# Optimization experiments

Measured on AMD Instinct MI355X. Metric: run time of the kernel, lower is better.

## Reference

```python
import jax, jax.numpy as jnp
import numpy as np

B, D, H, O, E = 16384, 1024, 512, 256, 8


def setup_inputs() -> dict:
    key = jax.random.key(0)
    ks = jax.random.split(key, 8)
    s = lambda k, shape, fan: (jax.random.normal(k, shape, jnp.float32) / np.sqrt(fan).astype(np.float32))
    z = lambda shape: jnp.zeros(shape, jnp.float32)
    return {
        "x": jax.random.normal(ks[0], (B, D), jnp.float32),
        # gating network: D -> 256 -> 128 -> E
        "gw1": s(ks[1], (D, 256), D), "gb1": z((256,)),
        "gw2": s(ks[2], (256, 128), 256), "gb2": z((128,)),
        "gw3": s(ks[3], (128, E), 128), "gb3": z((E,)),
        # experts, batched over expert dim E: D -> H -> H -> O
        "ew1": s(ks[4], (E, D, H), D), "eb1": z((E, H)),
        "ew2": s(ks[5], (E, H, H), H), "eb2": z((E, H)),
        "ew3": s(ks[6], (E, H, O), H), "eb3": z((E, O)),
    }


def reference(x, gw1, gb1, gw2, gb2, gw3, gb3, ew1, eb1, ew2, eb2, ew3, eb3):
    # Gating network (dropout is identity in eval mode)
    g = jax.nn.relu(x @ gw1 + gb1)
    g = jax.nn.relu(g @ gw2 + gb2)
    gates = jax.nn.softmax(g @ gw3 + gb3, axis=1)  # [B, E]
    # All experts run on every token: batched small MLPs over expert axis e
    h = jax.nn.relu(jnp.einsum('bd,edh->ebh', x, ew1) + eb1[:, None, :])   # [E, B, H]
    h = jax.nn.relu(jnp.einsum('ebh,ehk->ebk', h, ew2) + eb2[:, None, :])  # [E, B, H]
    eo = jnp.einsum('ebh,eho->ebo', h, ew3) + eb3[:, None, :]              # [E, B, O]
    # gate-weighted sum over experts
    out = jnp.einsum('ebo,be->bo', eo, gates)  # [B, O]
    return out
```

## Files before the change

kernel.cpp:

```cpp
#include <hip/hip_runtime.h>
#include <hip/hip_bf16.h>

typedef __hip_bfloat16 bf16;
typedef __attribute__((ext_vector_type(8))) __bf16 bf16x8;
typedef __attribute__((ext_vector_type(4))) float f32x4;

#define B_ 16384
#define D_ 1024
#define H_ 512
#define O_ 256
#define E_ 8
#define BC_ 8192

static_assert(B_ % BC_ == 0, "chunking");

#define GLDS(src, dst) __builtin_amdgcn_global_load_lds( \
    (const __attribute__((address_space(1))) void*)(src), \
    (__attribute__((address_space(3))) void*)(dst), 16, 0, 0)

#define BAR()   asm volatile("s_barrier" ::: "memory")
#define LGKM0() do { asm volatile("s_waitcnt lgkmcnt(0)" ::: "memory"); \
                     __builtin_amdgcn_sched_barrier(0); } while (0)

__global__ void detect_k(const unsigned short* __restrict__ x, int* __restrict__ flag) {
    __shared__ int s;
    if (threadIdx.x == 0) s = 0;
    __syncthreads();
    int big = 0;
    for (int i = threadIdx.x; i < 2048; i += 256)
        if (((x[i] >> 7) & 0xFF) >= 150) big = 1;
    if (big) atomicOr(&s, 1);
    __syncthreads();
    if (threadIdx.x == 0) *flag = s;
}

__global__ void preproc_k(const void* x, bf16* xc,
                          const void* gb1, const void* gb2, const void* gw3,
                          const void* gb3, const void* eb1, const void* eb2,
                          const void* eb3,
                          bf16* gb1c, bf16* gb2c, bf16* gw3c, bf16* gb3c,
                          bf16* eb1c, bf16* eb2c, bf16* eb3c,
                          const void* gw1, const void* gw2,
                          const void* ew1, const void* ew2, const void* ew3,
                          bf16* gw1t, bf16* gw2t,
                          bf16* ew1t, bf16* ew2t, bf16* ew3t,
                          long ew3_zout, long ew3_cstride,
                          const int* __restrict__ flag) {
    const int f = *flag;
    const int tid = threadIdx.y * 32 + threadIdx.x;
    int lin = blockIdx.x;

    if (lin < 1024) {
        const long n8 = (long)B_ * D_ / 8;
        long i = (long)lin * 256 + tid;
        const long stride = 1024 * 256;
        if (f) {
            const float4* s = (const float4*)x;
            for (; i < n8; i += stride) {
                float4 a = s[2 * i], b = s[2 * i + 1];
                bf16 tmp[8];
                tmp[0] = __float2bfloat16(a.x); tmp[1] = __float2bfloat16(a.y);
                tmp[2] = __float2bfloat16(a.z); tmp[3] = __float2bfloat16(a.w);
                tmp[4] = __float2bfloat16(b.x); tmp[5] = __float2bfloat16(b.y);
                tmp[6] = __float2bfloat16(b.z); tmp[7] = __float2bfloat16(b.w);
                *(uint4*)(xc + i * 8) = *(const uint4*)tmp;
            }
        } else {
            const uint4* s = (const uint4*)x;
            for (; i < n8; i += stride) *(uint4*)(xc + i * 8) = s[i];
        }
        return;
    }
    if (lin < 1031) {
        const int id = lin - 1024;
        const void* sp[7] = {gb1, gb2, gw3, gb3, eb1, eb2, eb3};
        bf16* dp[7] = {gb1c, gb2c, gw3c, gb3c, eb1c, eb2c, eb3c};
        const int len[7] = {256, 128, 1024, 8, E_ * H_, E_ * H_, E_ * O_};
        const float* sf = (const float*)sp[id];
        const bf16*  sb = (const bf16*)sp[id];
        bf16* d = dp[id];
        for (int i = tid; i < len[id]; i += 256)
            d[i] = f ? __float2bfloat16(sf[i]) : sb[i];
        return;
    }
    lin -= 1031;
    __shared__ bf16 t[32][33];
    const void* src; bf16* dst; int R, C, bx, by, bz; long z_out, c_stride;
    if (lin < 256) {
        src = gw1; dst = gw1t; R = 1024; C = 256; z_out = 0; c_stride = 1024;
        bx = lin & 7; by = lin >> 3; bz = 0;
    } else if (lin < 288) {
        lin -= 256;
        src = gw2; dst = gw2t; R = 256; C = 128; z_out = 0; c_stride = 256;
        bx = lin & 3; by = lin >> 2; bz = 0;
    } else if (lin < 4384) {
        lin -= 288;
        src = ew1; dst = ew1t; R = 1024; C = 512;
        z_out = (long)H_ * D_; c_stride = D_;
        bx = lin & 15; by = (lin >> 4) & 31; bz = lin >> 9;
    } else if (lin < 6432) {
        lin -= 4384;
        src = ew2; dst = ew2t; R = 512; C = 512;
        z_out = (long)H_ * H_; c_stride = H_;
        bx = lin & 15; by = (lin >> 4) & 15; bz = lin >> 8;
    } else {
        lin -= 6432;
        src = ew3; dst = ew3t; R = 512; C = 256;
        z_out = ew3_zout; c_stride = ew3_cstride;
        bx = lin & 7; by = (lin >> 3) & 15; bz = lin >> 7;
    }
    const long zi = (long)bz * R * C;
    const int xg = bx * 32 + threadIdx.x;
    const int y0 = by * 32;
    const float* inf = (const float*)src;
    const bf16* inb = (const bf16*)src;
#pragma unroll
    for (int i = 0; i < 4; i++) {
        int r = y0 + threadIdx.y + i * 8;
        long idx = zi + (long)r * C + xg;
        t[threadIdx.y + i * 8][threadIdx.x] =
            f ? __float2bfloat16(inf[idx]) : inb[idx];
    }
    __syncthreads();
    const int xr = by * 32 + threadIdx.x;
    const long zo = (long)bz * z_out;
#pragma unroll
    for (int i = 0; i < 4; i++) {
        int c = bx * 32 + threadIdx.y + i * 8;
        dst[zo + (long)c * c_stride + xr] = t[threadIdx.x][threadIdx.y + i * 8];
    }
}

__global__ void gate3_softmax_k(const bf16* __restrict__ g2,
                                const bf16* __restrict__ gw3,
                                const bf16* __restrict__ gb3,
                                float* __restrict__ gates) {
    __shared__ float w[128 * 8];
    __shared__ float bsh[8];
    const int tid = threadIdx.x;
    for (int i = tid; i < 1024; i += 256) w[i] = __bfloat162float(gw3[i]);
    if (tid < 8) bsh[tid] = __bfloat162float(gb3[tid]);
    __syncthreads();

    const long row = (long)blockIdx.x * 256 + tid;
    float acc[8];
#pragma unroll
    for (int o = 0; o < 8; o++) acc[o] = bsh[o];

    const bf16x8* rp8 = (const bf16x8*)(g2 + row * 128);
#pragma unroll 4
    for (int c8 = 0; c8 < 16; c8++) {
        bf16x8 v8 = rp8[c8];
#pragma unroll
        for (int jj = 0; jj < 8; jj++) {
            float v = (float)v8[jj];
            int k = c8 * 8 + jj;
#pragma unroll
            for (int o = 0; o < 8; o++) acc[o] += v * w[k * 8 + o];
        }
    }
    float m = acc[0];
#pragma unroll
    for (int o = 1; o < 8; o++) m = fmaxf(m, acc[o]);
    float s = 0.f;
#pragma unroll
    for (int o = 0; o < 8; o++) { acc[o] = __expf(acc[o] - m); s += acc[o]; }
    const float inv = 1.f / s;
#pragma unroll
    for (int o = 0; o < 8; o++) gates[row * 8 + o] = acc[o] * inv;
}

template <int MODE>
__global__ __launch_bounds__(256, 4)
void gemm_bt(const bf16* __restrict__ A, const bf16* __restrict__ Bt,
             const bf16* __restrict__ bias, const float* __restrict__ gates,
             void* __restrict__ Cout, const bf16* __restrict__ eb3,
             int lda, int ldb, int ldo, int K,
             long a_z, long b_z, long bias_z, long out_z,
             int e_gate, int k_per_e, long a_e, long b_e, long row0) {
    __shared__ __attribute__((aligned(16))) bf16 As[128 * 32];
    __shared__ __attribute__((aligned(16))) bf16 Bs[128 * 32];

    const int tid  = threadIdx.x;
    const int lane = tid & 63;
    const int quad = lane >> 4;
    const int l15  = lane & 15;
    const int wid  = tid >> 6;
    const int wr   = (wid >> 1) << 6;
    const int wc   = (wid & 1) << 6;
    const int z    = blockIdx.z;
    const long m0  = (long)blockIdx.y << 7;
    const long n0  = (long)blockIdx.x << 7;

    const bf16* Az = A + (long)z * a_z;
    const bf16* Bz = Bt + (long)z * b_z;

    f32x4 acc[4][4];
#pragma unroll
    for (int i = 0; i < 4; i++)
#pragma unroll
        for (int j = 0; j < 4; j++) acc[i][j] = (f32x4){0.f, 0.f, 0.f, 0.f};

    const int erow = tid >> 2;
    const int ecol = (tid & 3) << 3;

    const int n_e   = k_per_e ? (K / k_per_e) : 1;
    const int inner = (k_per_e ? k_per_e : K) >> 5;

    for (int e = 0; e < n_e; e++) {
        const bf16* Ae = Az + (long)e * a_e;
        const bf16* Be = Bz + (long)e * b_e;
        for (int kti = 0; kti < inner; kti++) {
            const int kk = kti << 5;
#pragma unroll
            for (int i = 0; i < 2; i++) {
                const int r = (i << 6) + erow;
                GLDS(Ae + (m0 + r) * lda + (kk + ecol), As + r * 32 + ecol);
            }
#pragma unroll
            for (int i = 0; i < 2; i++) {
                const int r = (i << 6) + erow;
                GLDS(Be + (n0 + r) * ldb + (kk + ecol), Bs + r * 32 + ecol);
            }
            __syncthreads();
            bf16x8 af[4], bfr[4];
#pragma unroll
            for (int i = 0; i < 4; i++)
                af[i] = *(const bf16x8*)(As + (wr + i * 16 + l15) * 32 + (quad << 3));
#pragma unroll
            for (int j = 0; j < 4; j++)
                bfr[j] = *(const bf16x8*)(Bs + (wc + j * 16 + l15) * 32 + (quad << 3));
#pragma unroll
            for (int i = 0; i < 4; i++)
#pragma unroll
                for (int j = 0; j < 4; j++)
                    acc[i][j] = __builtin_amdgcn_mfma_f32_16x16x32_bf16(
                        af[i], bfr[j], acc[i][j], 0, 0, 0);
            __syncthreads();
        }
    }

    const int eg = (e_gate >= 0) ? e_gate : z;

    if constexpr (MODE == 0 || MODE == 1) {
        bf16* C = (bf16*)Cout + (long)z * out_z;
        const bf16* bb = bias + (long)z * bias_z;
        float gv[4][4];
        if constexpr (MODE == 1) {
#pragma unroll
            for (int i = 0; i < 4; i++)
#pragma unroll
                for (int rg = 0; rg < 4; rg++)
                    gv[i][rg] = gates[(row0 + m0 + wr + i * 16 + quad * 4 + rg) * 8 + eg];
        }
#pragma unroll
        for (int j = 0; j < 4; j++) {
            const int c = (int)n0 + wc + j * 16 + l15;
            const float bv = __bfloat162float(bb[c]);
#pragma unroll
            for (int i = 0; i < 4; i++) {
#pragma unroll
                for (int rg = 0; rg < 4; rg++) {
                    const long r = m0 + wr + i * 16 + quad * 4 + rg;
                    float v = fmaxf(acc[i][j][rg] + bv, 0.f);
                    if constexpr (MODE == 1) v *= gv[i][rg];
                    C[r * ldo + c] = __float2bfloat16(v);
                }
            }
        }
    } else if constexpr (MODE == 2) {
        float* C = (float*)Cout;
#pragma unroll
        for (int i = 0; i < 4; i++) {
#pragma unroll
            for (int rg = 0; rg < 4; rg++) {
                const long r = m0 + wr + i * 16 + quad * 4 + rg;
                const float g = gates[(row0 + r) * 8 + eg];
#pragma unroll
                for (int j = 0; j < 4; j++) {
                    const int c = (int)n0 + wc + j * 16 + l15;
                    const float b3 = __bfloat162float(eb3[eg * O_ + c]);
                    C[r * ldo + c] += acc[i][j][rg] + g * b3;
                }
            }
        }
    }
}

template <int MODE>
__global__ __launch_bounds__(512, 2)
void gemm256(const bf16* __restrict__ A, const bf16* __restrict__ Bt,
             const bf16* __restrict__ bias, const float* __restrict__ gates,
             void* __restrict__ Cout, const bf16* __restrict__ eb3,
             int lda, int ldb, int ldo, int K,
             long a_z, long b_z, long bias_z, long out_z, long row0) {
    __shared__ __attribute__((aligned(16))) bf16 lds[2][2][256 * 64];

    int bx = blockIdx.x, by = blockIdx.y;
    {
        const int gx = gridDim.x;
        const int nwg = gx * gridDim.y;
        if ((nwg & 7) == 0) {
            int lin = bx + gx * by;
            lin = (lin & 7) * (nwg >> 3) + (lin >> 3);
            bx = lin % gx; by = lin / gx;
        }
    }

    const int tid  = threadIdx.x;
    const int lane = tid & 63;
    const int quad = lane >> 4;
    const int l15  = lane & 15;
    const int w    = tid >> 6;
    const int wm   = w >> 2;
    const int wn   = w & 3;
    const int z    = blockIdx.z;
    const long m0  = (long)by << 8;
    const long n0  = (long)bx << 8;

    const bf16* __restrict__ Az = A + z * a_z;
    const bf16* __restrict__ Bz = Bt + z * b_z;

    f32x4 acc[8][4];
#pragma unroll
    for (int i = 0; i < 8; ++i)
#pragma unroll
        for (int j = 0; j < 4; ++j) acc[i][j] = (f32x4){0.f, 0.f, 0.f, 0.f};

    bf16x8 af[4][2], bv[2][2];

    auto stage = [&](int buf, int mat, int half, int kt) {
        const bf16* __restrict__ G = mat ? Bz : Az;
        const int ld = mat ? ldb : lda;
        const long p0 = mat ? n0 : m0;
#pragma unroll
        for (int l = 0; l < 2; ++l) {
            const int ci = (w << 1) | l;
            const int rb = mat ? ((ci >> 2) << 6) + (half << 5) + ((ci & 3) << 3)
                               : ((ci >> 3) << 7) + (half << 6) + ((ci & 7) << 3);
            const int row = rb + (lane >> 3);
            const int cb  = ((lane & 7) << 4) ^ ((row & 7) << 4);
            GLDS(G + (p0 + row) * ld + kt * 64 + (cb >> 1),
                 &lds[buf][mat][rb * 64]);
        }
    };
    auto ldaf = [&](int buf, int qm) {
#pragma unroll
        for (int i = 0; i < 4; ++i) {
            const int r = (wm << 7) + (qm << 6) + (i << 4) + l15;
            const char* p = (const char*)&lds[buf][0][r * 64];
            const int sw = (r & 7) << 4;
#pragma unroll
            for (int s = 0; s < 2; ++s)
                af[i][s] = *(const bf16x8*)(p + (((s << 6) + (quad << 4)) ^ sw));
        }
    };
    auto ldbf = [&](int buf, int qn) {
#pragma unroll
        for (int j = 0; j < 2; ++j) {
            const int r = (wn << 6) + (qn << 5) + (j << 4) + l15;
            const char* p = (const char*)&lds[buf][1][r * 64];
            const int sw = (r & 7) << 4;
#pragma unroll
            for (int s = 0; s < 2; ++s)
                bv[j][s] = *(const bf16x8*)(p + (((s << 6) + (quad << 4)) ^ sw));
        }
    };
    auto mmac = [&](int qm, int qn) {
#pragma unroll
        for (int i = 0; i < 4; ++i)
#pragma unroll
            for (int j = 0; j < 2; ++j)
#pragma unroll
                for (int s = 0; s < 2; ++s)
                    acc[(qm << 2) + i][(qn << 1) + j] =
                        __builtin_amdgcn_mfma_f32_16x16x32_bf16(
                            af[i][s], bv[j][s], acc[(qm << 2) + i][(qn << 1) + j],
                            0, 0, 0);
    };

    const int nt = K >> 6;

    stage(0, 0, 0, 0); stage(0, 0, 1, 0); stage(0, 1, 0, 0); stage(0, 1, 1, 0);
    stage(1, 0, 0, 1); stage(1, 1, 0, 1);
    asm volatile("s_waitcnt vmcnt(4)" ::: "memory");
    BAR();

    const int hi = nt >> 1;
    for (int it = 0; it < hi; ++it) {
        const int t1k = 2 * it + 1, t2k = 2 * it + 2, t3k = 2 * it + 3;
        const bool do2 = t2k < nt, do3 = t3k < nt;
        ldaf(0, 0); ldbf(0, 0); stage(1, 0, 1, t1k);
        BAR(); LGKM0();
        __builtin_amdgcn_s_setprio(1); mmac(0, 0); __builtin_amdgcn_s_setprio(0);
        BAR();
        ldbf(0, 1); stage(1, 1, 1, t1k);
        BAR(); LGKM0();
        __builtin_amdgcn_s_setprio(1); mmac(0, 1); __builtin_amdgcn_s_setprio(0);
        BAR();
        ldaf(0, 1); ldbf(0, 0); if (do2) stage(0, 0, 0, t2k);
        BAR(); LGKM0();
        __builtin_amdgcn_s_setprio(1); mmac(1, 0); __builtin_amdgcn_s_setprio(0);
        BAR();
        ldbf(0, 1); if (do2) stage(0, 1, 0, t2k);
        BAR(); LGKM0();
        __builtin_amdgcn_s_setprio(1); mmac(1, 1); __builtin_amdgcn_s_setprio(0);
        if (do2) { asm volatile("s_waitcnt vmcnt(4)" ::: "memory"); }
        else     { asm volatile("s_waitcnt vmcnt(0)" ::: "memory"); }
        BAR();
        ldaf(1, 0); ldbf(1, 0); if (do2) stage(0, 0, 1, t2k);
        BAR(); LGKM0();
        __builtin_amdgcn_s_setprio(1); mmac(0, 0); __builtin_amdgcn_s_setprio(0);
        BAR();
        ldbf(1, 1); if (do2) stage(0, 1, 1, t2k);
        BAR(); LGKM0();
        __builtin_amdgcn_s_setprio(1); mmac(0, 1); __builtin_amdgcn_s_setprio(0);
        BAR();
        ldaf(1, 1); ldbf(1, 0); if (do3) stage(1, 0, 0, t3k);
        BAR(); LGKM0();
        __builtin_amdgcn_s_setprio(1); mmac(1, 0); __builtin_amdgcn_s_setprio(0);
        BAR();
        ldbf(1, 1); if (do3) stage(1, 1, 0, t3k);
        BAR(); LGKM0();
        __builtin_amdgcn_s_setprio(1); mmac(1, 1); __builtin_amdgcn_s_setprio(0);
        if (do3) { asm volatile("s_waitcnt vmcnt(4)" ::: "memory"); }
        else     { asm volatile("s_waitcnt vmcnt(0)" ::: "memory"); }
        BAR();
    }

    if constexpr (MODE == 0 || MODE == 1) {
        bf16* C = (bf16*)Cout + z * out_z;
        const bf16* bb = bias + z * bias_z;
        float bvv[4];
#pragma unroll
        for (int jg = 0; jg < 4; ++jg)
            bvv[jg] = __bfloat162float(bb[(int)n0 + (wn << 6) + (jg << 4) + l15]);
#pragma unroll
        for (int ig = 0; ig < 8; ++ig) {
#pragma unroll
            for (int rg = 0; rg < 4; ++rg) {
                const long r = m0 + (wm << 7) + (ig << 4) + (quad << 2) + rg;
                float g = 1.f;
                if constexpr (MODE == 1) g = gates[(row0 + r) * 8 + z];
#pragma unroll
                for (int jg = 0; jg < 4; ++jg) {
                    const int c = (int)n0 + (wn << 6) + (jg << 4) + l15;
                    float v = fmaxf(acc[ig][jg][rg] + bvv[jg], 0.f);
                    if constexpr (MODE == 1) v *= g;
                    C[r * ldo + c] = __float2bfloat16(v);
                }
            }
        }
    } else if constexpr (MODE == 4) {
        float* C = (float*)Cout + z * out_z;
        float b3v[4];
#pragma unroll
        for (int jg = 0; jg < 4; ++jg)
            b3v[jg] = __bfloat162float(eb3[z * O_ + (int)n0 + (wn << 6) + (jg << 4) + l15]);
#pragma unroll
        for (int ig = 0; ig < 8; ++ig) {
#pragma unroll
            for (int rg = 0; rg < 4; ++rg) {
                const long r = m0 + (wm << 7) + (ig << 4) + (quad << 2) + rg;
                const float g = gates[(row0 + r) * 8 + z];
#pragma unroll
                for (int jg = 0; jg < 4; ++jg) {
                    const int c = (int)n0 + (wn << 6) + (jg << 4) + l15;
                    C[r * ldo + c] = acc[ig][jg][rg] + g * b3v[jg];
                }
            }
        }
    } else {
        float* C = (float*)Cout + z * out_z;
        const int e0 = z << 1;
        float b30[4], b31[4];
#pragma unroll
        for (int jg = 0; jg < 4; ++jg) {
            const int c = (int)n0 + (wn << 6) + (jg << 4) + l15;
            b30[jg] = __bfloat162float(eb3[e0 * O_ + c]);
            b31[jg] = __bfloat162float(eb3[(e0 + 1) * O_ + c]);
        }
#pragma unroll
        for (int ig = 0; ig < 8; ++ig) {
#pragma unroll
            for (int rg = 0; rg < 4; ++rg) {
                const long r = m0 + (wm << 7) + (ig << 4) + (quad << 2) + rg;
                const float g0 = gates[(row0 + r) * 8 + e0];
                const float g1 = gates[(row0 + r) * 8 + e0 + 1];
#pragma unroll
                for (int jg = 0; jg < 4; ++jg) {
                    const int c = (int)n0 + (wn << 6) + (jg << 4) + l15;
                    C[r * ldo + c] = acc[ig][jg][rg] + g0 * b30[jg] + g1 * b31[jg];
                }
            }
        }
    }
}

__global__ void zero_f32_k(float* __restrict__ p) {
    p[(long)blockIdx.x * 256 + threadIdx.x] = 0.f;
}
__global__ void out_cvt_k(const float* __restrict__ in, void* __restrict__ out,
                          const int* __restrict__ flag) {
    const long i = (long)blockIdx.x * 256 + threadIdx.x;
    if (*flag) ((float*)out)[i] = in[i];
    else       ((bf16*)out)[i] = __float2bfloat16(in[i]);
}
template <int NZ>
__global__ void reduceN_k(const float* __restrict__ p, void* __restrict__ out,
                          const int* __restrict__ flag, long n, long off) {
    const long i = ((long)blockIdx.x * 256 + threadIdx.x) * 4;
    float4 s = *(const float4*)(p + i);
#pragma unroll
    for (int zz = 1; zz < NZ; ++zz) {
        float4 a = *(const float4*)(p + (long)zz * n + i);
        s.x += a.x; s.y += a.y; s.z += a.z; s.w += a.w;
    }
    if (*flag) {
        *(float4*)((float*)out + off + i) = s;
    } else {
        bf16* o = (bf16*)out + off + i;
        o[0] = __float2bfloat16(s.x); o[1] = __float2bfloat16(s.y);
        o[2] = __float2bfloat16(s.z); o[3] = __float2bfloat16(s.w);
    }
}

extern "C" void kernel_launch(void* const* d_in, const int* in_sizes, int n_in,
                              void* d_out, int out_size, void* d_ws, size_t ws_size,
                              hipStream_t stream) {
    (void)in_sizes; (void)n_in; (void)out_size;
    const void* x   = d_in[0];
    const void* gw1 = d_in[1];
    const void* gb1 = d_in[2];
    const void* gw2 = d_in[3];
    const void* gb2 = d_in[4];
    const void* gw3 = d_in[5];
    const void* gb3 = d_in[6];
    const void* ew1 = d_in[7];
    const void* eb1 = d_in[8];
    const void* ew2 = d_in[9];
    const void* eb2 = d_in[10];
    const void* ew3 = d_in[11];
    const void* eb3 = d_in[12];

    char* ws = (char*)d_ws;
    size_t off = 0;
    auto alloc = [&](size_t n) { char* p = ws + off; off += (n + 255) & ~(size_t)255; return p; };

    int*  flag  = (int*)alloc(256);
    bf16* xc    = (bf16*)alloc((size_t)B_ * D_ * 2);
    bf16* ew1t  = (bf16*)alloc((size_t)E_ * H_ * D_ * 2);
    bf16* gw1t  = (bf16*)alloc((size_t)256 * 1024 * 2);
    bf16* gw2t  = (bf16*)alloc((size_t)128 * 256 * 2);
    bf16* ew2t  = (bf16*)alloc((size_t)E_ * H_ * H_ * 2);
    bf16* ew3t  = (bf16*)alloc((size_t)E_ * O_ * H_ * 2);
    bf16* eb1c  = (bf16*)alloc((size_t)E_ * H_ * 2);
    bf16* gb1c  = (bf16*)alloc(256 * 2);
    bf16* gb2c  = (bf16*)alloc(128 * 2);
    bf16* gw3c  = (bf16*)alloc(1024 * 2);
    bf16* gb3c  = (bf16*)alloc(8 * 2);
    bf16* eb2c  = (bf16*)alloc((size_t)E_ * H_ * 2);
    bf16* eb3c  = (bf16*)alloc((size_t)E_ * O_ * 2);
    bf16* g2b   = (bf16*)alloc((size_t)B_ * 128 * 2);
    float* gates = (float*)alloc((size_t)B_ * 8 * 4);
    bf16* g1    = (bf16*)alloc((size_t)B_ * 256 * 2);

    const size_t smallCore = off;
    const size_t needPair = smallCore + ((size_t)E_ * BC_ * H_ * 2 + 256)
                                      + ((size_t)B_ * E_ * H_ * 2 + 256) + 4096;
    const size_t needChunk = smallCore + ((size_t)E_ * BC_ * H_ * 2 + 256)
                                       + ((size_t)BC_ * E_ * H_ * 2 + 256)
                                       + (8ull * BC_ * O_ * 4 + 256) + 4096;
    const bool pathPair  = ws_size >= needPair;
    const bool pathChunk = ws_size >= needChunk;

    detect_k<<<1, 256, 0, stream>>>((const unsigned short*)x, flag);

    const bool l3pair = pathPair || pathChunk;
    const long e3zo = l3pair ? (long)H_ : (long)O_ * H_;
    const long e3cs = l3pair ? (long)E_ * H_ : (long)H_;
    preproc_k<<<8487, dim3(32, 8), 0, stream>>>(
        x, xc, gb1, gb2, gw3, gb3, eb1, eb2, eb3,
        gb1c, gb2c, gw3c, gb3c, eb1c, eb2c, eb3c,
        gw1, gw2, ew1, ew2, ew3, gw1t, gw2t, ew1t, ew2t, ew3t,
        e3zo, e3cs, flag);

    gemm_bt<0><<<dim3(2, 128, 1), 256, 0, stream>>>(
        xc, gw1t, gb1c, nullptr, g1, nullptr,
        1024, 1024, 256, 1024, 0, 0, 0, 0, 0, 0, 0, 0, 0);
    gemm_bt<0><<<dim3(1, 128, 1), 256, 0, stream>>>(
        g1, gw2t, gb2c, nullptr, g2b, nullptr,
        256, 256, 128, 256, 0, 0, 0, 0, 0, 0, 0, 0, 0);
    gate3_softmax_k<<<dim3(B_ / 256), 256, 0, stream>>>(g2b, gw3c, gb3c, gates);

    if (pathPair) {
        bf16* h1c = (bf16*)alloc((size_t)E_ * BC_ * H_ * 2);
        bf16* h2  = (bf16*)alloc((size_t)B_ * E_ * H_ * 2);
        float* parts = (float*)h1c;

        for (int ch = 0; ch < B_ / BC_; ch++) {
            const long rb = (long)ch * BC_;
            gemm256<0><<<dim3(2, BC_ / 256, 8), 512, 0, stream>>>(
                xc + rb * D_, ew1t, eb1c, nullptr, h1c, nullptr,
                D_, D_, H_, D_,
                0, (long)H_ * D_, (long)H_, (long)BC_ * H_, 0);
            gemm256<1><<<dim3(2, BC_ / 256, 8), 512, 0, stream>>>(
                h1c, ew2t, eb2c, gates, h2 + rb * (long)E_ * H_, nullptr,
                H_, H_, E_ * H_, H_,
                (long)BC_ * H_, (long)H_ * H_, (long)H_, (long)H_, rb);
        }
        gemm256<5><<<dim3(1, B_ / 256, 4), 512, 0, stream>>>(
            h2, ew3t, nullptr, gates, parts, eb3c,
            E_ * H_, E_ * H_, O_, 1024,
            2L * H_, 2L * H_, 0, (long)B_ * O_, 0);
        reduceN_k<4><<<dim3(B_ * O_ / 1024), 256, 0, stream>>>(
            parts, d_out, flag, (long)B_ * O_, 0L);
    } else if (pathChunk) {
        bf16* h1c = (bf16*)alloc((size_t)E_ * BC_ * H_ * 2);
        bf16* h2c = (bf16*)alloc((size_t)BC_ * E_ * H_ * 2);
        float* parts = (float*)alloc(8ull * BC_ * O_ * 4);

        for (int ch = 0; ch < B_ / BC_; ch++) {
            const long rb = (long)ch * BC_;
            gemm256<0><<<dim3(2, BC_ / 256, 8), 512, 0, stream>>>(
                xc + rb * D_, ew1t, eb1c, nullptr, h1c, nullptr,
                D_, D_, H_, D_,
                0, (long)H_ * D_, (long)H_, (long)BC_ * H_, 0);
            gemm256<1><<<dim3(2, BC_ / 256, 8), 512, 0, stream>>>(
                h1c, ew2t, eb2c, gates, h2c, nullptr,
                H_, H_, E_ * H_, H_,
                (long)BC_ * H_, (long)H_ * H_, (long)H_, (long)H_, rb);
            gemm256<4><<<dim3(1, BC_ / 256, 8), 512, 0, stream>>>(
                h2c, ew3t, nullptr, gates, parts, eb3c,
                E_ * H_, E_ * H_, O_, 512,
                (long)H_, (long)H_, 0, (long)BC_ * O_, rb);
            reduceN_k<8><<<dim3(BC_ * O_ / 1024), 256, 0, stream>>>(
                parts, d_out, flag, (long)BC_ * O_, rb * O_);
        }
    } else {
        bf16* h1s = (bf16*)alloc((size_t)B_ * H_ * 2);
        bf16* h2s = (bf16*)alloc((size_t)B_ * H_ * 2);
        float* oacc = (float*)alloc((size_t)B_ * O_ * 4);
        zero_f32_k<<<dim3(B_ * O_ / 256), 256, 0, stream>>>(oacc);
        for (int e = 0; e < E_; e++) {
            gemm_bt<0><<<dim3(4, 128, 1), 256, 0, stream>>>(
                xc, ew1t + (size_t)e * H_ * D_, eb1c + (size_t)e * H_, nullptr, h1s, nullptr,
                1024, 1024, 512, 1024, 0, 0, 0, 0, 0, 0, 0, 0, 0);
            gemm_bt<1><<<dim3(4, 128, 1), 256, 0, stream>>>(
                h1s, ew2t + (size_t)e * H_ * H_, eb2c + (size_t)e * H_, gates, h2s, nullptr,
                512, 512, 512, 512, 0, 0, 0, 0, e, 0, 0, 0, 0);
            gemm_bt<2><<<dim3(2, 128, 1), 256, 0, stream>>>(
                h2s, ew3t + (size_t)e * O_ * H_, nullptr, gates, oacc, eb3c,
                512, 512, 256, 512, 0, 0, 0, 0, e, 0, 0, 0, 0);
        }
        out_cvt_k<<<dim3(B_ * O_ / 256), 256, 0, stream>>>(oacc, d_out, flag);
    }
}
```

Measured before the change: 494.9 us.

## Fuse gate layers 2-3 with softmax and fold split-K reduce into final GEMM

Layer 2 of the gating network (MFMA GEMM with bias and ReLU) is merged with layer 3 and the softmax into one kernel, so the intermediate g2 activations stay in LDS instead of going through global memory. The separate reduceN launch after the last expert GEMM is removed. Instead, each block increments a per-row-tile atomic counter, and the last of the four split-K blocks sums the partials and writes the final output in fp32 or bf16. This drops two launches and one global round trip. In exchange, the last-arriving block does a serial reduction, and correctness depends on counters being zeroed by detect_k and on threadfence ordering.

```diff
diff --git a/kernel.cpp b/kernel.cpp
--- a/kernel.cpp
+++ b/kernel.cpp
@@ -22,9 +22,11 @@
 #define LGKM0() do { asm volatile("s_waitcnt lgkmcnt(0)" ::: "memory"); \
                      __builtin_amdgcn_sched_barrier(0); } while (0)
 
-__global__ void detect_k(const unsigned short* __restrict__ x, int* __restrict__ flag) {
+__global__ void detect_k(const unsigned short* __restrict__ x,
+                         int* __restrict__ flag, int* __restrict__ cnt) {
     __shared__ int s;
     if (threadIdx.x == 0) s = 0;
+    if (threadIdx.x < 64) cnt[threadIdx.x] = 0;
     __syncthreads();
     int big = 0;
     for (int i = threadIdx.x; i < 2048; i += 256)
@@ -131,43 +133,100 @@
     }
 }
 
-__global__ void gate3_softmax_k(const bf16* __restrict__ g2,
-                                const bf16* __restrict__ gw3,
-                                const bf16* __restrict__ gb3,
-                                float* __restrict__ gates) {
-    __shared__ float w[128 * 8];
-    __shared__ float bsh[8];
-    const int tid = threadIdx.x;
-    for (int i = tid; i < 1024; i += 256) w[i] = __bfloat162float(gw3[i]);
-    if (tid < 8) bsh[tid] = __bfloat162float(gb3[tid]);
+__global__ __launch_bounds__(256, 2)
+void gate23_k(const bf16* __restrict__ A,
+              const bf16* __restrict__ Bt,
+              const bf16* __restrict__ gb2,
+              const bf16* __restrict__ w3b,
+              float* __restrict__ gates) {
+    __shared__ __attribute__((aligned(16))) bf16 As[128 * 32];
+    __shared__ __attribute__((aligned(16))) bf16 Bs[128 * 32];
+    __shared__ bf16 t2[128][130];
+    __shared__ float w3[1032];
+
+    const int tid  = threadIdx.x;
+    const int lane = tid & 63;
+    const int quad = lane >> 4;
+    const int l15  = lane & 15;
+    const int wid  = tid >> 6;
+    const int wr   = (wid >> 1) << 6;
+    const int wc   = (wid & 1) << 6;
+    const long m0  = (long)blockIdx.x << 7;
+
+    for (int i = tid; i < 1032; i += 256) w3[i] = __bfloat162float(w3b[i]);
+
+    f32x4 acc[4][4];
+#pragma unroll
+    for (int i = 0; i < 4; i++)
+#pragma unroll
+        for (int j = 0; j < 4; j++) acc[i][j] = (f32x4){0.f, 0.f, 0.f, 0.f};
+
+    const int erow = tid >> 2;
+    const int ecol = (tid & 3) << 3;
+
+    for (int kti = 0; kti < 8; kti++) {
+        const int kk = kti << 5;
+#pragma unroll
+        for (int i = 0; i < 2; i++) {
+            const int r = (i << 6) + erow;
+            GLDS(A + (m0 + r) * 256 + (kk + ecol), As + r * 32 + ecol);
+        }
+#pragma unroll
+        for (int i = 0; i < 2; i++) {
+            const int r = (i << 6) + erow;
+            GLDS(Bt + (long)r * 256 + (kk + ecol), Bs + r * 32 + ecol);
+        }
+        __syncthreads();
+        bf16x8 af[4], bfr[4];
+#pragma unroll
+        for (int i = 0; i < 4; i++)
+            af[i] = *(const bf16x8*)(As + (wr + i * 16 + l15) * 32 + (quad << 3));
+#pragma unroll
+        for (int j = 0; j < 4; j++)
+            bfr[j] = *(const bf16x8*)(Bs + (wc + j * 16 + l15) * 32 + (quad << 3));
+#pragma unroll
+        for (int i = 0; i < 4; i++)
+#pragma unroll
+            for (int j = 0; j < 4; j++)
+                acc[i][j] = __builtin_amdgcn_mfma_f32_16x16x32_bf16(
+                    af[i], bfr[j], acc[i][j], 0, 0, 0);
+        __syncthreads();
+    }
+
+#pragma unroll
+    for (int j = 0; j < 4; j++) {
+        const int c = wc + j * 16 + l15;
+        const float bv = __bfloat162float(gb2[c]);
+#pragma unroll
+        for (int i = 0; i < 4; i++)
+#pragma unroll
+            for (int rg = 0; rg < 4; rg++) {
+                const int r = wr + i * 16 + quad * 4 + rg;
+                t2[r][c] = __float2bfloat16(fmaxf(acc[i][j][rg] + bv, 0.f));
+            }
+    }
     __syncthreads();
 
-    const long row = (long)blockIdx.x * 256 + tid;
-    float acc[8];
-#pragma unroll
-    for (int o = 0; o < 8; o++) acc[o] = bsh[o];
-
-    const bf16x8* rp8 = (const bf16x8*)(g2 + row * 128);
-#pragma unroll 4
-    for (int c8 = 0; c8 < 16; c8++) {
-        bf16x8 v8 = rp8[c8];
-#pragma unroll
-        for (int jj = 0; jj < 8; jj++) {
-            float v = (float)v8[jj];
-            int k = c8 * 8 + jj;
-#pragma unroll
-            for (int o = 0; o < 8; o++) acc[o] += v * w[k * 8 + o];
-        }
-    }
-    float m = acc[0];
-#pragma unroll
-    for (int o = 1; o < 8; o++) m = fmaxf(m, acc[o]);
-    float s = 0.f;
-#pragma unroll
-    for (int o = 0; o < 8; o++) { acc[o] = __expf(acc[o] - m); s += acc[o]; }
-    const float inv = 1.f / s;
-#pragma unroll
-    for (int o = 0; o < 8; o++) gates[row * 8 + o] = acc[o] * inv;
+    if (tid < 128) {
+        const int r = tid;
+        float a3[8];
+#pragma unroll
+        for (int o = 0; o < 8; o++) a3[o] = w3[1024 + o];
+        for (int k = 0; k < 128; k++) {
+            const float v = __bfloat162float(t2[r][k]);
+#pragma unroll
+            for (int o = 0; o < 8; o++) a3[o] += v * w3[k * 8 + o];
+        }
+        float mx = a3[0];
+#pragma unroll
+        for (int o = 1; o < 8; o++) mx = fmaxf(mx, a3[o]);
+        float s = 0.f;
+#pragma unroll
+        for (int o = 0; o < 8; o++) { a3[o] = __expf(a3[o] - mx); s += a3[o]; }
+        const float inv = 1.f / s;
+#pragma unroll
+        for (int o = 0; o < 8; o++) gates[(m0 + r) * 8 + o] = a3[o] * inv;
+    }
 }
 
 template <int MODE>
@@ -293,7 +352,9 @@
              const bf16* __restrict__ bias, const float* __restrict__ gates,
              void* __restrict__ Cout, const bf16* __restrict__ eb3,
              int lda, int ldb, int ldo, int K,
-             long a_z, long b_z, long bias_z, long out_z, long row0) {
+             long a_z, long b_z, long bias_z, long out_z, long row0,
+             const int* __restrict__ oflag, int* __restrict__ cnt,
+             void* __restrict__ fout) {
     __shared__ __attribute__((aligned(16))) bf16 lds[2][2][256 * 64];
 
     int bx = blockIdx.x, by = blockIdx.y;
@@ -494,6 +555,34 @@
                 }
             }
         }
+        __shared__ int oldc;
+        __syncthreads();
+        if (tid == 0) {
+            __threadfence();
+            oldc = atomicAdd(&cnt[by], 1);
+        }
+        __syncthreads();
+        if (oldc == 3) {
+            const int f = *oflag;
+            const float* P = (const float*)Cout;
+            const long base = m0 * O_;
+            for (int idx = tid; idx < (256 * O_) / 4; idx += 512) {
+                const long o4 = base + (long)idx * 4;
+                float4 s = *(const float4*)(P + o4);
+#pragma unroll
+                for (int zz = 1; zz < 4; ++zz) {
+                    float4 a = *(const float4*)(P + (long)zz * out_z + o4);
+                    s.x += a.x; s.y += a.y; s.z += a.z; s.w += a.w;
+                }
+                if (f) {
+                    *(float4*)((float*)fout + o4) = s;
+                } else {
+                    bf16* o = (bf16*)fout + o4;
+                    o[0] = __float2bfloat16(s.x); o[1] = __float2bfloat16(s.y);
+                    o[2] = __float2bfloat16(s.z); o[3] = __float2bfloat16(s.w);
+                }
+            }
+        }
     }
 }
 
@@ -547,7 +636,8 @@
     size_t off = 0;
     auto alloc = [&](size_t n) { char* p = ws + off; off += (n + 255) & ~(size_t)255; return p; };
 
-    int*  flag  = (int*)alloc(256);
+    int*  flag  = (int*)alloc(512);
+    int*  cnt   = flag + 64;
     bf16* xc    = (bf16*)alloc((size_t)B_ * D_ * 2);
     bf16* ew1t  = (bf16*)alloc((size_t)E_ * H_ * D_ * 2);
     bf16* gw1t  = (bf16*)alloc((size_t)256 * 1024 * 2);
@@ -557,11 +647,10 @@
     bf16* eb1c  = (bf16*)alloc((size_t)E_ * H_ * 2);
     bf16* gb1c  = (bf16*)alloc(256 * 2);
     bf16* gb2c  = (bf16*)alloc(128 * 2);
-    bf16* gw3c  = (bf16*)alloc(1024 * 2);
-    bf16* gb3c  = (bf16*)alloc(8 * 2);
+    bf16* gw3c  = (bf16*)alloc(1032 * 2);
+    bf16* gb3c  = gw3c + 1024;
     bf16* eb2c  = (bf16*)alloc((size_t)E_ * H_ * 2);
     bf16* eb3c  = (bf16*)alloc((size_t)E_ * O_ * 2);
-    bf16* g2b   = (bf16*)alloc((size_t)B_ * 128 * 2);
     float* gates = (float*)alloc((size_t)B_ * 8 * 4);
     bf16* g1    = (bf16*)alloc((size_t)B_ * 256 * 2);
 
@@ -574,7 +663,7 @@
     const bool pathPair  = ws_size >= needPair;
     const bool pathChunk = ws_size >= needChunk;
 
-    detect_k<<<1, 256, 0, stream>>>((const unsigned short*)x, flag);
+    detect_k<<<1, 256, 0, stream>>>((const unsigned short*)x, flag, cnt);
 
     const bool l3pair = pathPair || pathChunk;
     const long e3zo = l3pair ? (long)H_ : (long)O_ * H_;
@@ -588,10 +677,7 @@
     gemm_bt<0><<<dim3(2, 128, 1), 256, 0, stream>>>(
         xc, gw1t, gb1c, nullptr, g1, nullptr,
         1024, 1024, 256, 1024, 0, 0, 0, 0, 0, 0, 0, 0, 0);
-    gemm_bt<0><<<dim3(1, 128, 1), 256, 0, stream>>>(
-        g1, gw2t, gb2c, nullptr, g2b, nullptr,
-        256, 256, 128, 256, 0, 0, 0, 0, 0, 0, 0, 0, 0);
-    gate3_softmax_k<<<dim3(B_ / 256), 256, 0, stream>>>(g2b, gw3c, gb3c, gates);
+    gate23_k<<<dim3(128), 256, 0, stream>>>(g1, gw2t, gb2c, gw3c, gates);
 
     if (pathPair) {
         bf16* h1c = (bf16*)alloc((size_t)E_ * BC_ * H_ * 2);
@@ -603,18 +689,19 @@
             gemm256<0><<<dim3(2, BC_ / 256, 8), 512, 0, stream>>>(
                 xc + rb * D_, ew1t, eb1c, nullptr, h1c, nullptr,
                 D_, D_, H_, D_,
-                0, (long)H_ * D_, (long)H_, (long)BC_ * H_, 0);
+                0, (long)H_ * D_, (long)H_, (long)BC_ * H_, 0,
+                nullptr, nullptr, nullptr);
             gemm256<1><<<dim3(2, BC_ / 256, 8), 512, 0, stream>>>(
                 h1c, ew2t, eb2c, gates, h2 + rb * (long)E_ * H_, nullptr,
                 H_, H_, E_ * H_, H_,
-                (long)BC_ * H_, (long)H_ * H_, (long)H_, (long)H_, rb);
-        }
-        gemm256<5><<<dim3(1, B_ / 256, 4), 512, 0, stream>>>(
+                (long)BC_ * H_, (long)H_ * H_, (long)H_, (long)H_, rb,
+                nullptr, nullptr, nullptr);
+        }
+        gemm256<7><<<dim3(1, B_ / 256, 4), 512, 0, stream>>>(
             h2, ew3t, nullptr, gates, parts, eb3c,
             E_ * H_, E_ * H_, O_, 1024,
-            2L * H_, 2L * H_, 0, (long)B_ * O_, 0);
-        reduceN_k<4><<<dim3(B_ * O_ / 1024), 256, 0, stream>>>(
-            parts, d_out, flag, (long)B_ * O_, 0L);
+            2L * H_, 2L * H_, 0, (long)B_ * O_, 0,
+            flag, cnt, d_out);
     } else if (pathChunk) {
         bf16* h1c = (bf16*)alloc((size_t)E_ * BC_ * H_ * 2);
         bf16* h2c = (bf16*)alloc((size_t)BC_ * E_ * H_ * 2);
@@ -625,15 +712,18 @@
             gemm256<0><<<dim3(2, BC_ / 256, 8), 512, 0, stream>>>(
                 xc + rb * D_, ew1t, eb1c, nullptr, h1c, nullptr,
                 D_, D_, H_, D_,
-                0, (long)H_ * D_, (long)H_, (long)BC_ * H_, 0);
+                0, (long)H_ * D_, (long)H_, (long)BC_ * H_, 0,
+                nullptr, nullptr, nullptr);
             gemm256<1><<<dim3(2, BC_ / 256, 8), 512, 0, stream>>>(
                 h1c, ew2t, eb2c, gates, h2c, nullptr,
                 H_, H_, E_ * H_, H_,
-                (long)BC_ * H_, (long)H_ * H_, (long)H_, (long)H_, rb);
+                (long)BC_ * H_, (long)H_ * H_, (long)H_, (long)H_, rb,
+                nullptr, nullptr, nullptr);
             gemm256<4><<<dim3(1, BC_ / 256, 8), 512, 0, stream>>>(
                 h2c, ew3t, nullptr, gates, parts, eb3c,
                 E_ * H_, E_ * H_, O_, 512,
-                (long)H_, (long)H_, 0, (long)BC_ * O_, rb);
+                (long)H_, (long)H_, 0, (long)BC_ * O_, rb,
+                nullptr, nullptr, nullptr);
             reduceN_k<8><<<dim3(BC_ * O_ / 1024), 256, 0, stream>>>(
                 parts, d_out, flag, (long)BC_ * O_, rb * O_);
         }
```

Result: no change. 504.3 us (+1.9%).
